# Kernel optimization log

Measured on AMD Instinct MI355X. Metric: run time of the kernel, lower is better.

Reference implementation:

```python
import jax, jax.numpy as jnp
import numpy as np

IN_DIM = 256
QK_DIM = IN_DIM // 8  # 32
NCLS = 19
B, H, W = 2, 64, 64


def conv3x3(x, w, b):
    # x: [B,C,H,W], w: [O,I,3,3] -> SAME padding, stride 1 (= pad=1 in torch)
    y = jax.lax.conv_general_dilated(x, w, (1, 1), 'SAME',
                                     dimension_numbers=('NCHW', 'OIHW', 'NCHW'))
    return y + b[None, :, None, None]


def setup_inputs() -> dict:
    key = jax.random.key(0)
    ks = jax.random.split(key, 20)
    s = 0.05
    inp = {
        'x': jax.random.normal(ks[0], (B, IN_DIM, H, W), jnp.float32),
        'modal_mask': jax.random.uniform(ks[1], (B, NCLS, H, W), jnp.float32),
        'amodal_mask': jax.random.uniform(ks[2], (B, NCLS, H, W), jnp.float32),
        'w_mp': jax.random.normal(ks[3], (NCLS, IN_DIM, 3, 3), jnp.float32) * s,
        'b_mp': jnp.zeros((NCLS,), jnp.float32),
        'w_ap': jax.random.normal(ks[4], (NCLS, IN_DIM, 3, 3), jnp.float32) * s,
        'b_ap': jnp.zeros((NCLS,), jnp.float32),
        'w_q': jax.random.normal(ks[5], (QK_DIM, IN_DIM + NCLS, 3, 3), jnp.float32) * s,
        'b_q': jnp.zeros((QK_DIM,), jnp.float32),
        'w_k': jax.random.normal(ks[6], (QK_DIM, IN_DIM + NCLS, 3, 3), jnp.float32) * s,
        'b_k': jnp.zeros((QK_DIM,), jnp.float32),
        'w_v': jax.random.normal(ks[7], (IN_DIM, IN_DIM, 3, 3), jnp.float32) * s,
        'b_v': jnp.zeros((IN_DIM,), jnp.float32),
        'w_comp': jax.random.normal(ks[8], (IN_DIM, IN_DIM + 2 * NCLS, 3, 3), jnp.float32) * s,
        'b_comp': jnp.zeros((IN_DIM,), jnp.float32),
        'w_out': jax.random.normal(ks[9], (IN_DIM, 3 * IN_DIM, 3, 3), jnp.float32) * s,
        'b_out': jnp.zeros((IN_DIM,), jnp.float32),
        # SELayer(in_dim, reduction=8): Linear(c, c//8, bias=False), Linear(c//8, c, bias=False)
        'w_se1': jax.random.normal(ks[10], (IN_DIM // 8, IN_DIM), jnp.float32) * s,
        'w_se2': jax.random.normal(ks[11], (IN_DIM, IN_DIM // 8), jnp.float32) * s,
    }
    return inp


def reference(x, modal_mask, amodal_mask, w_mp, b_mp, w_ap, b_ap, w_q, b_q,
              w_k, b_k, w_v, b_v, w_comp, b_comp, w_out, b_out, w_se1, w_se2):
    b, c, h, w = x.shape
    n = h * w
    # masks already at (h, w): nearest interpolate is identity
    modal_x = conv3x3(x, w_mp, b_mp) * modal_mask
    amodal_x = conv3x3(x, w_ap, b_ap) * amodal_mask
    inp = jnp.concatenate([x, modal_x, amodal_x], axis=1)
    out = conv3x3(inp, w_comp, b_comp)
    # SE layer
    y = out.mean(axis=(2, 3))                                # [b, c]
    y = jax.nn.sigmoid(jax.nn.relu(y @ w_se1.T) @ w_se2.T)   # [b, c]
    out_a = out * y[:, :, None, None]
    # dual-softmax spatial attention
    q = conv3x3(jnp.concatenate([x, modal_mask], axis=1), w_q, b_q).reshape(b, QK_DIM, n)
    k = conv3x3(jnp.concatenate([x, amodal_mask], axis=1), w_k, b_k).reshape(b, QK_DIM, n)
    v = conv3x3(x, w_v, b_v).reshape(b, c, n)
    energy = jnp.einsum('bdn,bdm->bnm', q, k)                # [b, n, n]
    attn = jax.nn.softmax(energy, axis=-1)                   # softmax over keys
    attn_t = jax.nn.softmax(energy, axis=1)                  # softmax over queries (of E^T rows)
    # out_b = bmm(v, attn^T); out_c = bmm(v, softmax(E^T,-1)^T)
    out_b = jnp.einsum('bcn,bmn->bcm', v, attn).reshape(b, c, h, w)
    out_c = jnp.einsum('bcn,bnm->bcm', v, attn_t).reshape(b, c, h, w)
    out = jnp.concatenate([out_a, out_b, out_c], axis=1)
    return conv3x3(out, w_out, b_out)
```

## Files before the change

kernel.cpp:

```cpp
#include <hip/hip_runtime.h>
#include <math.h>

#define HW 4096
#define IMG 64
#define PIX66 (66 * 66)

typedef short short8 __attribute__((ext_vector_type(8)));
typedef float f32x4 __attribute__((ext_vector_type(4)));

__device__ __forceinline__ unsigned short f2bf(float f) {
    unsigned int u = __float_as_uint(f);
    u += 0x7fff + ((u >> 16) & 1);
    return (unsigned short)(u >> 16);
}
__device__ __forceinline__ float bf2f(unsigned short h) {
    return __uint_as_float(((unsigned int)h) << 16);
}
__device__ __forceinline__ unsigned int pkbf(float a, float b) {
    unsigned int ua = __float_as_uint(a) + 0x8000u;
    unsigned int ub = __float_as_uint(b) + 0x8000u;
    return __builtin_amdgcn_perm(ub, ua, 0x07060302u);
}

__device__ __forceinline__ void gll16(const unsigned short* g, unsigned short* l) {
    __builtin_amdgcn_global_load_lds(
        (const __attribute__((address_space(1))) unsigned int*)(g),
        (__attribute__((address_space(3))) unsigned int*)(l), 16, 0, 0);
}

__device__ __forceinline__ int pxor(int pix) { return (pix ^ (pix >> 2)) & 3; }
__device__ __forceinline__ int p32o(int pix, int c) {
    return pix * 32 + ((((c >> 3) ^ pxor(pix)) & 3) << 3) + (c & 7);
}

struct WtJob {
    const float* w;
    unsigned short* dh;
    unsigned short* dl;
    int OC, OCpad, C0, K0pad, C1, Ktot;
};

__global__ __launch_bounds__(256) void k_wt_all(WtJob J0, WtJob J1, WtJob J2,
                                                WtJob J3, WtJob J4, WtJob J5,
                                                WtJob J6) {
    WtJob J;
    switch (blockIdx.y) {
        case 0: J = J0; break;
        case 1: J = J1; break;
        case 2: J = J2; break;
        case 3: J = J3; break;
        case 4: J = J4; break;
        case 5: J = J5; break;
        default: J = J6; break;
    }
    int idx = blockIdx.x * 256 + threadIdx.x;
    int KS = J.Ktot >> 5;
    int n = 9 * KS * J.OCpad * 32;
    if (idx >= n) return;
    int kk = idx & 31;
    int rest = idx >> 5;
    int oc = rest % J.OCpad;
    rest /= J.OCpad;
    int kg = rest % KS;
    int tap = rest / KS;
    int k = kg * 32 + kk;
    float v = 0.f;
    if (oc < J.OC) {
        int ic = -1;
        if (k < J.C0) ic = k;
        else if (k >= J.K0pad && (k - J.K0pad) < J.C1) ic = J.C0 + (k - J.K0pad);
        if (ic >= 0) v = J.w[((size_t)oc * (J.C0 + J.C1) + ic) * 9 + tap];
    }
    unsigned short hi = f2bf(v);
    J.dh[idx] = hi;
    if (J.dl) J.dl[idx] = f2bf(v - bf2f(hi));
}

__global__ __launch_bounds__(256) void k_build_x(const float* __restrict__ x,
                                                 unsigned short* __restrict__ xh,
                                                 unsigned short* __restrict__ xl,
                                                 unsigned short* __restrict__ ipad) {
    int b = blockIdx.z, c0 = blockIdx.y * 64, p0 = blockIdx.x * 64;
    __shared__ float s[64][65];
    int t = threadIdx.x;
    for (int i = t; i < 4096; i += 256) {
        int c = i >> 6, p = i & 63;
        s[p][c] = x[((size_t)b * 256 + c0 + c) * HW + p0 + p];
    }
    __syncthreads();
    for (int i = t; i < 4096; i += 256) {
        int c = i & 63, p = i >> 6;
        float f = s[p][c];
        unsigned short hi = f2bf(f);
        unsigned short lo = f2bf(f - bf2f(hi));
        int pp = p0 + p;
        int y = pp >> 6, xx = pp & 63;
        int pix = (y + 1) * 66 + xx + 1;
        int C = c0 + c;
        size_t ix = (size_t)(b * 8 + (C >> 5)) * (PIX66 * 32) + p32o(pix, C & 31);
        xh[ix] = hi;
        xl[ix] = lo;
        ipad[(size_t)(b * 10 + (C >> 5)) * (PIX66 * 32) + p32o(pix, C & 31)] = hi;
    }
}

__global__ __launch_bounds__(256) void k_build_mask2(
    const float* __restrict__ m0, const float* __restrict__ m1,
    unsigned short* __restrict__ d0h, unsigned short* __restrict__ d0l,
    unsigned short* __restrict__ d1h, unsigned short* __restrict__ d1l) {
    const float* m = blockIdx.y ? m1 : m0;
    unsigned short* dh = blockIdx.y ? d1h : d0h;
    unsigned short* dl = blockIdx.y ? d1l : d0l;
    int idx = blockIdx.x * 256 + threadIdx.x;
    int c = idx & 31;
    int p = (idx >> 5) & 4095;
    int b = idx >> 17;
    float f = (c < 19) ? m[((size_t)b * 19 + c) * HW + p] : 0.f;
    unsigned short hi = f2bf(f);
    int y = p >> 6, xx = p & 63;
    int pix = (y + 1) * 66 + xx + 1;
    dh[(size_t)b * (PIX66 * 32) + p32o(pix, c)] = hi;
    dl[(size_t)b * (PIX66 * 32) + p32o(pix, c)] = f2bf(f - bf2f(hi));
}

struct DJob {
    const unsigned short* s1h;
    const unsigned short* s1l;
    const unsigned short* wth;
    const unsigned short* wtl;
    const float* bias;
    unsigned short* d1;
    unsigned short* d2;
    const float* mask;
    int chBase;
    int mode;
    int split;
    int KS1;
};

__global__ __launch_bounds__(128, 2) void conv_direct_all(
    const unsigned short* __restrict__ s0h, const unsigned short* __restrict__ s0l,
    DJob j0, DJob j1, DJob j2, DJob j3) {
    DJob J;
    switch (blockIdx.y) {
        case 0: J = j0; break;
        case 1: J = j1; break;
        case 2: J = j2; break;
        default: J = j3; break;
    }
    const int KS0 = 8;
    int KS = KS0 + J.KS1;
    int ST = 9 * KS;
    int b = blockIdx.z;
    int t = threadIdx.x, w = t >> 6, l = t & 63, quad = l >> 4, ln = l & 15;
    int pBase = blockIdx.x * 64 + w * 32;

    int padpix[2];
#pragma unroll
    for (int tn = 0; tn < 2; ++tn) {
        int p = pBase + tn * 16 + ln;
        padpix[tn] = ((p >> 6) + 1) * 66 + (p & 63) + 1;
    }
    size_t aoff[2];
#pragma unroll
    for (int tm = 0; tm < 2; ++tm) aoff[tm] = (size_t)(tm * 16 + ln) * 32 + quad * 8;

    const unsigned short* S0H = s0h + (size_t)b * KS0 * PIX66 * 32;
    const unsigned short* S0L = s0l + (size_t)b * KS0 * PIX66 * 32;
    const unsigned short* S1H = J.KS1 ? J.s1h + (size_t)b * PIX66 * 32
                                      : (const unsigned short*)0;
    const unsigned short* S1L = J.KS1 ? J.s1l + (size_t)b * PIX66 * 32
                                      : (const unsigned short*)0;

    f32x4 acc[2][2];
#pragma unroll
    for (int i = 0; i < 2; ++i)
#pragma unroll
        for (int j = 0; j < 2; ++j) acc[i][j] = (f32x4){0.f, 0.f, 0.f, 0.f};

    int tap = 0, kg = 0;
    auto adv = [&]() { if (++kg == KS) { kg = 0; ++tap; } };
    auto loadStep = [&](int ltap, int lkg, short8* bh, short8* bl, short8* ah,
                        short8* al) {
        int d3 = ltap / 3;
        int dpix = (d3 - 1) * 66 + (ltap - d3 * 3 - 1);
        const unsigned short* SpH;
        const unsigned short* SpL;
        long plane;
        if (lkg < KS0) {
            SpH = S0H; SpL = S0L; plane = (long)lkg * PIX66 * 32;
        } else {
            SpH = S1H; SpL = S1L; plane = 0;
        }
#pragma unroll
        for (int tn = 0; tn < 2; ++tn) {
            int pix2 = padpix[tn] + dpix;
            long off = plane + (long)pix2 * 32 + (((quad ^ pxor(pix2)) & 3) << 3);
            bh[tn] = *(const short8*)(SpH + off);
            if (J.split) bl[tn] = *(const short8*)(SpL + off);
        }
        const unsigned short* WTh = J.wth + (size_t)(ltap * KS + lkg) * 32 * 32;
        ah[0] = *(const short8*)(WTh + aoff[0]);
        ah[1] = *(const short8*)(WTh + aoff[1]);
        if (J.split) {
            const unsigned short* WTl = J.wtl + (size_t)(ltap * KS + lkg) * 32 * 32;
            al[0] = *(const short8*)(WTl + aoff[0]);
            al[1] = *(const short8*)(WTl + aoff[1]);
        }
    };

    short8 BH[2][2], AH[2][2], BL[2][2], AL[2][2];
#pragma unroll
    for (int u = 0; u < 2; ++u) { loadStep(tap, kg, BH[u], BL[u], AH[u], AL[u]); adv(); }

    for (int s = 0; s < ST; s += 2) {
#pragma unroll
        for (int u = 0; u < 2; ++u) {
            if (s + u < ST) {
#pragma unroll
                for (int tm = 0; tm < 2; ++tm)
#pragma unroll
                    for (int tn = 0; tn < 2; ++tn) {
                        acc[tm][tn] = __builtin_amdgcn_mfma_f32_16x16x32_bf16(
                            AH[u][tm], BH[u][tn], acc[tm][tn], 0, 0, 0);
                        if (J.split) {
                            acc[tm][tn] = __builtin_amdgcn_mfma_f32_16x16x32_bf16(
                                AL[u][tm], BH[u][tn], acc[tm][tn], 0, 0, 0);
                            acc[tm][tn] = __builtin_amdgcn_mfma_f32_16x16x32_bf16(
                                AH[u][tm], BL[u][tn], acc[tm][tn], 0, 0, 0);
                        }
                    }
                if (s + u + 2 < ST) { loadStep(tap, kg, BH[u], BL[u], AH[u], AL[u]); adv(); }
            }
        }
    }

#pragma unroll
    for (int tm = 0; tm < 2; ++tm) {
#pragma unroll
        for (int r = 0; r < 4; ++r) {
            int oc = tm * 16 + quad * 4 + r;
#pragma unroll
            for (int tn = 0; tn < 2; ++tn) {
                int p = pBase + tn * 16 + ln;
                if (J.mode == 1) {
                    if (oc < 19) {
                        float v = (acc[tm][tn][r] + J.bias[oc]) *
                                  J.mask[((size_t)b * 19 + oc) * HW + p];
                        int ch = J.chBase + oc;
                        J.d1[(size_t)(b * 10 + (ch >> 5)) * (PIX66 * 32) +
                             p32o(padpix[tn], ch & 31)] = f2bf(v);
                    }
                } else {
                    float v = acc[tm][tn][r] + J.bias[oc];
                    unsigned short hi = f2bf(v);
                    J.d1[((size_t)b * HW + p) * 32 + oc] = hi;
                    J.d2[((size_t)b * HW + p) * 32 + oc] = f2bf(v - bf2f(hi));
                }
            }
        }
    }
}

struct LJob {
    const unsigned short* src;
    const unsigned short* wt;
    float* dstf;
    int KS;
    int nseg;
    int doSum;
};

__global__ __launch_bounds__(128, 3) void conv_lds(LJob j0, LJob j1, int ocgPerJob,
                                                   float* __restrict__ ybuf) {
    int jy = blockIdx.y;
    LJob J = (jy >= ocgPerJob) ? j1 : j0;
    int ocBase = ((jy >= ocgPerJob) ? jy - ocgPerJob : jy) * 64;
    int z = blockIdx.z;
    int b = z & 1, seg = z >> 1;
    int kgPer = J.KS / J.nseg;
    int kgBeg = seg * kgPer, kgEnd = kgBeg + kgPer;
    int ry = blockIdx.x * 2;
    int t = threadIdx.x, w = t >> 6, l = t & 63, quad = l >> 4, ln = l & 15;

    __shared__ unsigned short sB[2][264 * 32];

    const unsigned short* S = J.src + (size_t)b * J.KS * PIX66 * 32;
    const size_t bStageBase = (size_t)(ry * 66) * 32;

    f32x4 acc[4][4];
#pragma unroll
    for (int i = 0; i < 4; ++i)
#pragma unroll
        for (int j = 0; j < 4; ++j) acc[i][j] = (f32x4){0.f, 0.f, 0.f, 0.f};

    {
        const unsigned short* gB = S + (size_t)kgBeg * PIX66 * 32 + bStageBase;
        for (int i = t; i < 1056; i += 128) gll16(gB + (size_t)i * 8, sB[0] + (size_t)i * 8);
    }

    for (int kg = kgBeg; kg < kgEnd; ++kg) {
        int cur = (kg - kgBeg) & 1;
        __syncthreads();
        if (kg + 1 < kgEnd) {
            const unsigned short* gB = S + (size_t)(kg + 1) * PIX66 * 32 + bStageBase;
            for (int i = t; i < 1056; i += 128)
                gll16(gB + (size_t)i * 8, sB[cur ^ 1] + (size_t)i * 8);
        }
        const unsigned short* sBc = sB[cur];
#pragma unroll
        for (int tap = 0; tap < 9; ++tap) {
            const unsigned short* gA =
                J.wt + ((size_t)(tap * J.KS + kg) * 256 + ocBase) * 32;
            int dy = tap / 3 - 1, dx = tap % 3 - 1;
            int lpBase = (1 + w + dy) * 66 + 1 + dx;
            short8 bf[4], af[4];
#pragma unroll
            for (int tn = 0; tn < 4; ++tn) {
                int lp = lpBase + tn * 16 + ln;
                int P = ry * 66 + lp;
                bf[tn] = *(const short8*)(sBc + (size_t)lp * 32 +
                                          (((quad ^ pxor(P)) & 3) << 3));
            }
#pragma unroll
            for (int tm = 0; tm < 4; ++tm)
                af[tm] = *(const short8*)(gA + (size_t)(tm * 16 + ln) * 32 + quad * 8);
#pragma unroll
            for (int tm = 0; tm < 4; ++tm)
#pragma unroll
                for (int tn = 0; tn < 4; ++tn)
                    acc[tm][tn] = __builtin_amdgcn_mfma_f32_16x16x32_bf16(
                        af[tm], bf[tn], acc[tm][tn], 0, 0, 0);
        }
    }

    int prow = ry + w;
#pragma unroll
    for (int tm = 0; tm < 4; ++tm) {
#pragma unroll
        for (int r = 0; r < 4; ++r) {
            int oc = ocBase + tm * 16 + quad * 4 + r;
            float msum = 0.f;
#pragma unroll
            for (int tn = 0; tn < 4; ++tn) {
                int px = tn * 16 + ln;
                J.dstf[((size_t)z * 256 + oc) * HW + prow * 64 + px] = acc[tm][tn][r];
                msum += acc[tm][tn][r];
            }
            if (J.doSum) {
#pragma unroll
                for (int off = 8; off; off >>= 1) msum += __shfl_down(msum, off, 16);
                if (ln == 0) atomicAdd(&ybuf[b * 256 + oc], msum);
            }
        }
    }
}

__global__ __launch_bounds__(256) void vt_combine(const float* __restrict__ part,
                                                  const float* __restrict__ bias,
                                                  unsigned short* __restrict__ vt) {
    int idx = blockIdx.x * 256 + threadIdx.x;
    int p = idx & 4095;
    int oc = (idx >> 12) & 255;
    int b = idx >> 20;
    float v = part[((size_t)b * 256 + oc) * HW + p] +
              part[((size_t)(2 + b) * 256 + oc) * HW + p] + bias[oc];
    int prow = p >> 6, px = p & 63;
    int jc = ((px >> 3) ^ (oc & 7)) & 7;
    vt[(((size_t)b * 64 + prow) * 256 + oc) * 64 + jc * 8 + (px & 7)] = f2bf(v);
}

__global__ __launch_bounds__(256) void comp_combine(const float* __restrict__ part,
                                                    const float* __restrict__ bias,
                                                    const float* __restrict__ sc,
                                                    unsigned short* __restrict__ catN) {
    int idx = blockIdx.x * 256 + threadIdx.x;
    int p = idx & 4095;
    int oc = (idx >> 12) & 255;
    int b = idx >> 20;
    float v = (part[((size_t)b * 256 + oc) * HW + p] +
               part[((size_t)(2 + b) * 256 + oc) * HW + p] + bias[oc]) *
              sc[b * 256 + oc];
    int prow = p >> 6, px = p & 63;
    int pix = (prow + 1) * 66 + px + 1;
    catN[(size_t)(b * 24 + (oc >> 5)) * (PIX66 * 32) + p32o(pix, oc & 31)] = f2bf(v);
}

__global__ __launch_bounds__(256) void out_combine(const float* __restrict__ part,
                                                   const float* __restrict__ bias,
                                                   float* __restrict__ outp) {
    int idx = blockIdx.x * 256 + threadIdx.x;
    int p = idx & 4095;
    int oc = (idx >> 12) & 255;
    int b = idx >> 20;
    float v = part[((size_t)(0 + b) * 256 + oc) * HW + p] +
              part[((size_t)(2 + b) * 256 + oc) * HW + p] +
              part[((size_t)(4 + b) * 256 + oc) * HW + p] +
              part[((size_t)(6 + b) * 256 + oc) * HW + p] + bias[oc];
    outp[((size_t)b * 256 + oc) * HW + p] = v;
}

__global__ __launch_bounds__(512, 4) void flash_attn(
    const unsigned short* __restrict__ qt_h, const unsigned short* __restrict__ qt_l,
    const unsigned short* __restrict__ kt_h, const unsigned short* __restrict__ kt_l,
    const unsigned short* __restrict__ vt,
    float* __restrict__ pO, float* __restrict__ pm, float* __restrict__ pl) {
    int seg = blockIdx.y >> 1, mode = blockIdx.y & 1, b = blockIdx.z;
    size_t qkoff = (size_t)b * HW * 32;
    const unsigned short* Qh = (mode ? kt_h : qt_h) + qkoff;
    const unsigned short* Ql = (mode ? kt_l : qt_l) + qkoff;
    const unsigned short* Kh = (mode ? qt_h : kt_h) + qkoff;
    const unsigned short* Kl = (mode ? qt_l : kt_l) + qkoff;
    const unsigned short* Vt = vt + (size_t)b * 64 * 256 * 64;

    int t = threadIdx.x, w = t >> 6, l = t & 63, quad = l >> 4, ln = l & 15;
    int pg = w & 1, ch = w >> 1;
    int p0 = blockIdx.x * 64, pw = pg * 32;
    int cb = ch * 64;
    bool soft = (ch == (pg ? 3 : 0));

    __shared__ unsigned short sV[256 * 64];
    __shared__ unsigned short sP[64 * 68];
    __shared__ float sAl[64];

    short8 qbh[2], qbl[2];
    if (soft) {
#pragma unroll
        for (int pn = 0; pn < 2; ++pn) {
            size_t off = (size_t)(p0 + pw + pn * 16 + ln) * 32 + quad * 8;
            qbh[pn] = *(const short8*)(Qh + off);
            qbl[pn] = *(const short8*)(Ql + off);
        }
    }

    float m_run[2] = {-3.0e38f, -3.0e38f};
    float l_run[2] = {0.f, 0.f};
    f32x4 accO[4][2];
#pragma unroll
    for (int cs = 0; cs < 4; ++cs)
#pragma unroll
        for (int pn = 0; pn < 2; ++pn) accO[cs][pn] = (f32x4){0.f, 0.f, 0.f, 0.f};

    int jbBeg = seg * (HW / 2);
    for (int jb = jbBeg; jb < jbBeg + HW / 2; jb += 64) {
        __syncthreads();
        {
            const unsigned short* gV = Vt + (size_t)(jb >> 6) * (256 * 64);
#pragma unroll
            for (int i = 0; i < 4; ++i)
                gll16(gV + (size_t)(t + 512 * i) * 8, sV + (size_t)(t + 512 * i) * 8);
        }
        if (soft) {
            f32x4 sacc[2][4];
#pragma unroll
            for (int pn = 0; pn < 2; ++pn)
#pragma unroll
                for (int jj = 0; jj < 4; ++jj) sacc[pn][jj] = (f32x4){0.f, 0.f, 0.f, 0.f};
#pragma unroll
            for (int jj = 0; jj < 4; ++jj) {
                size_t off = (size_t)(jb + 16 * jj + ln) * 32 + quad * 8;
                short8 kh = *(const short8*)(Kh + off);
                short8 kr = *(const short8*)(Kl + off);
#pragma unroll
                for (int pn = 0; pn < 2; ++pn) {
                    sacc[pn][jj] = __builtin_amdgcn_mfma_f32_16x16x32_bf16(
                        kh, qbh[pn], sacc[pn][jj], 0, 0, 0);
                    sacc[pn][jj] = __builtin_amdgcn_mfma_f32_16x16x32_bf16(
                        kh, qbl[pn], sacc[pn][jj], 0, 0, 0);
                    sacc[pn][jj] = __builtin_amdgcn_mfma_f32_16x16x32_bf16(
                        kr, qbh[pn], sacc[pn][jj], 0, 0, 0);
                }
            }
#pragma unroll
            for (int pn = 0; pn < 2; ++pn) {
                float tmx = -3.0e38f;
#pragma unroll
                for (int jj = 0; jj < 4; ++jj)
#pragma unroll
                    for (int r = 0; r < 4; ++r) tmx = fmaxf(tmx, sacc[pn][jj][r]);
                tmx = fmaxf(tmx, __shfl_xor(tmx, 16));
                tmx = fmaxf(tmx, __shfl_xor(tmx, 32));
                float mnew = fmaxf(m_run[pn], tmx);
                float alpha = __expf(m_run[pn] - mnew);
                m_run[pn] = mnew;
                float psum = 0.f;
#pragma unroll
                for (int jj = 0; jj < 4; ++jj) {
                    float e0 = __expf(sacc[pn][jj][0] - mnew);
                    float e1 = __expf(sacc[pn][jj][1] - mnew);
                    float e2 = __expf(sacc[pn][jj][2] - mnew);
                    float e3 = __expf(sacc[pn][jj][3] - mnew);
                    psum += (e0 + e1) + (e2 + e3);
                    uint2 pk;
                    pk.x = pkbf(e0, e1);
                    pk.y = pkbf(e2, e3);
                    *(uint2*)(sP + (size_t)(pw + pn * 16 + ln) * 68 + jj * 16 +
                              quad * 4) = pk;
                }
                psum += __shfl_xor(psum, 16);
                psum += __shfl_xor(psum, 32);
                l_run[pn] = l_run[pn] * alpha + psum;
                if (quad == 0) sAl[pw + pn * 16 + ln] = alpha;
            }
        }
        __syncthreads();
        float al0 = sAl[pw + ln];
        float al1 = sAl[pw + 16 + ln];
#pragma unroll
        for (int cs = 0; cs < 4; ++cs) { accO[cs][0] *= al0; accO[cs][1] *= al1; }
#pragma unroll
        for (int j2 = 0; j2 < 2; ++j2) {
            short8 pb0 = *(const short8*)(sP + (size_t)(pw + ln) * 68 + j2 * 32 +
                                          quad * 8);
            short8 pb1 = *(const short8*)(sP + (size_t)(pw + 16 + ln) * 68 + j2 * 32 +
                                          quad * 8);
#pragma unroll
            for (int cs = 0; cs < 4; ++cs) {
                int c = cb + cs * 16 + ln;
                short8 va = *(const short8*)(
                    sV + (size_t)c * 64 + ((((j2 * 4 + quad) ^ (c & 7)) & 7) << 3));
                accO[cs][0] = __builtin_amdgcn_mfma_f32_16x16x32_bf16(
                    va, pb0, accO[cs][0], 0, 0, 0);
                accO[cs][1] = __builtin_amdgcn_mfma_f32_16x16x32_bf16(
                    va, pb1, accO[cs][1], 0, 0, 0);
            }
        }
    }

    int idx4 = (seg * 2 + mode) * 2 + b;
#pragma unroll
    for (int pn = 0; pn < 2; ++pn) {
        int p = p0 + pw + pn * 16 + ln;
        if (soft && quad == 0) {
            pm[(size_t)idx4 * HW + p] = m_run[pn];
            pl[(size_t)idx4 * HW + p] = l_run[pn];
        }
#pragma unroll
        for (int cs = 0; cs < 4; ++cs)
#pragma unroll
            for (int r = 0; r < 4; ++r) {
                int c = cb + cs * 16 + quad * 4 + r;
                pO[((size_t)idx4 * 256 + c) * HW + p] = accO[cs][pn][r];
            }
    }
}

__global__ __launch_bounds__(256) void attn_combine(const float* __restrict__ pO,
                                                    const float* __restrict__ pm,
                                                    const float* __restrict__ pl,
                                                    unsigned short* __restrict__ catN) {
    int b = blockIdx.z, mode = blockIdx.y;
    int t = threadIdx.x;
    int p = blockIdx.x * 64 + (t & 63);
    int c0 = (t >> 6) * 64;
    int i0 = mode * 2 + b;
    int i1 = 4 + mode * 2 + b;
    float m0 = pm[(size_t)i0 * HW + p], m1 = pm[(size_t)i1 * HW + p];
    float l0 = pl[(size_t)i0 * HW + p], l1 = pl[(size_t)i1 * HW + p];
    float M = fmaxf(m0, m1);
    float e0 = __expf(m0 - M), e1 = __expf(m1 - M);
    float inv = 1.f / (l0 * e0 + l1 * e1);
    e0 *= inv;
    e1 *= inv;
    int y = p >> 6, x = p & 63;
    int pix = (y + 1) * 66 + x + 1;
    for (int c = c0; c < c0 + 64; ++c) {
        float v = pO[((size_t)i0 * 256 + c) * HW + p] * e0 +
                  pO[((size_t)i1 * 256 + c) * HW + p] * e1;
        int cf = 256 + mode * 256 + c;
        catN[(size_t)(b * 24 + (cf >> 5)) * (PIX66 * 32) + p32o(pix, cf & 31)] = f2bf(v);
    }
}

__global__ __launch_bounds__(256) void se_mlp_kernel(const float* __restrict__ y,
                                                     const float* __restrict__ bcomp,
                                                     const float* __restrict__ w1,
                                                     const float* __restrict__ w2,
                                                     float* __restrict__ sc) {
    int b = blockIdx.x, t = threadIdx.x;
    __shared__ float sy[256], sh[32];
    sy[t] = y[b * 256 + t] * (1.f / 4096.f) + bcomp[t];
    __syncthreads();
    if (t < 32) {
        float s = 0.f;
        for (int c = 0; c < 256; ++c) s = fmaf(w1[t * 256 + c], sy[c], s);
        sh[t] = fmaxf(s, 0.f);
    }
    __syncthreads();
    float s = 0.f;
#pragma unroll
    for (int h = 0; h < 32; ++h) s = fmaf(w2[t * 32 + h], sh[h], s);
    sc[b * 256 + t] = 1.f / (1.f + __expf(-s));
}

extern "C" void kernel_launch(void* const* d_in, const int* in_sizes, int n_in,
                              void* d_out, int out_size, void* d_ws, size_t ws_size,
                              hipStream_t stream) {
    const float* x      = (const float*)d_in[0];
    const float* mmask  = (const float*)d_in[1];
    const float* amask  = (const float*)d_in[2];
    const float* w_mp   = (const float*)d_in[3];
    const float* b_mp   = (const float*)d_in[4];
    const float* w_ap   = (const float*)d_in[5];
    const float* b_ap   = (const float*)d_in[6];
    const float* w_q    = (const float*)d_in[7];
    const float* b_q    = (const float*)d_in[8];
    const float* w_k    = (const float*)d_in[9];
    const float* b_k    = (const float*)d_in[10];
    const float* w_v    = (const float*)d_in[11];
    const float* b_v    = (const float*)d_in[12];
    const float* w_comp = (const float*)d_in[13];
    const float* b_comp = (const float*)d_in[14];
    const float* w_out  = (const float*)d_in[15];
    const float* b_out  = (const float*)d_in[16];
    const float* w_se1  = (const float*)d_in[17];
    const float* w_se2  = (const float*)d_in[18];

    unsigned short* us = (unsigned short*)d_ws;
    size_t o = 0;
    unsigned short* xpad_hi = us + o; o += (size_t)2 * 8 * PIX66 * 32;
    unsigned short* xpad_lo = us + o; o += (size_t)2 * 8 * PIX66 * 32;
    unsigned short* mq_hi   = us + o; o += (size_t)2 * PIX66 * 32;
    unsigned short* mq_lo   = us + o; o += (size_t)2 * PIX66 * 32;
    unsigned short* ma_hi   = us + o; o += (size_t)2 * PIX66 * 32;
    unsigned short* ma_lo   = us + o; o += (size_t)2 * PIX66 * 32;
    unsigned short* ipad    = us + o; o += (size_t)2 * 10 * PIX66 * 32;
    unsigned short* catN    = us + o; o += (size_t)2 * 24 * PIX66 * 32;
    size_t zeroBytes = o * sizeof(unsigned short);
    unsigned short* wt_mp = us + o; o += (size_t)9 * 8 * 32 * 32;
    unsigned short* wt_ap = us + o; o += (size_t)9 * 8 * 32 * 32;
    unsigned short* wt_qh = us + o; o += (size_t)9 * 9 * 32 * 32;
    unsigned short* wt_ql = us + o; o += (size_t)9 * 9 * 32 * 32;
    unsigned short* wt_kh = us + o; o += (size_t)9 * 9 * 32 * 32;
    unsigned short* wt_kl = us + o; o += (size_t)9 * 9 * 32 * 32;
    unsigned short* wt_v  = us + o; o += (size_t)9 * 8 * 256 * 32;
    unsigned short* wt_cp = us + o; o += (size_t)9 * 10 * 256 * 32;
    unsigned short* wt_ot = us + o; o += (size_t)9 * 24 * 256 * 32;
    unsigned short* qt_h  = us + o; o += (size_t)2 * HW * 32;
    unsigned short* qt_l  = us + o; o += (size_t)2 * HW * 32;
    unsigned short* kt_h  = us + o; o += (size_t)2 * HW * 32;
    unsigned short* kt_l  = us + o; o += (size_t)2 * HW * 32;
    unsigned short* vt    = us + o; o += (size_t)2 * 64 * 256 * 64;
    float* fp = (float*)(us + o);
    size_t fo = 0;
    float* pAtt = fp + fo; fo += (size_t)8 * 256 * HW;
    float* pmb  = fp + fo; fo += (size_t)8 * HW;
    float* plb  = fp + fo; fo += (size_t)8 * HW;
    float* pOut = fp + fo; fo += (size_t)8 * 256 * HW;
    float* pV   = fp + fo; fo += (size_t)4 * 256 * HW;
    float* pC   = fp + fo; fo += (size_t)4 * 256 * HW;
    float* ybuf = fp + fo; fo += 512;
    float* sbuf = fp + fo; fo += 512;
    size_t need = o * sizeof(unsigned short) + fo * sizeof(float);
    if (ws_size < need) return;

    float* outp = (float*)d_out;

    hipMemsetAsync(us, 0, zeroBytes, stream);
    hipMemsetAsync(ybuf, 0, 512 * sizeof(float), stream);

    WtJob W0{w_mp,   wt_mp, (unsigned short*)0, 19, 32, 256, 256, 0, 256};
    WtJob W1{w_ap,   wt_ap, (unsigned short*)0, 19, 32, 256, 256, 0, 256};
    WtJob W2{w_q,    wt_qh, wt_ql,             32, 32, 256, 256, 19, 288};
    WtJob W3{w_k,    wt_kh, wt_kl,             32, 32, 256, 256, 19, 288};
    WtJob W4{w_v,    wt_v,  (unsigned short*)0, 256, 256, 256, 256, 0, 256};
    WtJob W5{w_comp, wt_cp, (unsigned short*)0, 256, 256, 294, 320, 0, 320};
    WtJob W6{w_out,  wt_ot, (unsigned short*)0, 256, 256, 768, 768, 0, 768};
    k_wt_all<<<dim3((9 * 24 * 256 * 32 + 255) / 256, 7), 256, 0, stream>>>(
        W0, W1, W2, W3, W4, W5, W6);

    k_build_x<<<dim3(64, 4, 2), 256, 0, stream>>>(x, xpad_hi, xpad_lo, ipad);
    k_build_mask2<<<dim3(1024, 2), 256, 0, stream>>>(mmask, amask, mq_hi, mq_lo,
                                                     ma_hi, ma_lo);

    const unsigned short* NUS = (const unsigned short*)0;
    unsigned short* NUSo = (unsigned short*)0;
    float* NF = (float*)0;

    DJob dm{NUS, NUS, wt_mp, NUS, b_mp, ipad, NUSo, mmask, 256, 1, 0, 0};
    DJob da{NUS, NUS, wt_ap, NUS, b_ap, ipad, NUSo, amask, 275, 1, 0, 0};
    DJob dq{mq_hi, mq_lo, wt_qh, wt_ql, b_q, qt_h, qt_l, NF, 0, 2, 1, 1};
    DJob dk{ma_hi, ma_lo, wt_kh, wt_kl, b_k, kt_h, kt_l, NF, 0, 2, 1, 1};
    conv_direct_all<<<dim3(64, 4, 2), 128, 0, stream>>>(xpad_hi, xpad_lo, dm, da, dq, dk);

    LJob lv{xpad_hi, wt_v, pV, 8, 2, 0};
    LJob lc{ipad, wt_cp, pC, 10, 2, 1};
    conv_lds<<<dim3(32, 8, 4), 128, 0, stream>>>(lv, lc, 4, ybuf);

    se_mlp_kernel<<<2, 256, 0, stream>>>(ybuf, b_comp, w_se1, w_se2, sbuf);
    vt_combine<<<8192, 256, 0, stream>>>(pV, b_v, vt);
    comp_combine<<<8192, 256, 0, stream>>>(pC, b_comp, sbuf, catN);

    flash_attn<<<dim3(64, 4, 2), 512, 0, stream>>>(qt_h, qt_l, kt_h, kt_l, vt,
                                                   pAtt, pmb, plb);
    attn_combine<<<dim3(64, 2, 2), 256, 0, stream>>>(pAtt, pmb, plb, catN);

    LJob lo{catN, wt_ot, pOut, 24, 4, 0};
    conv_lds<<<dim3(32, 4, 8), 128, 0, stream>>>(lo, lo, 4, NF);
    out_combine<<<8192, 256, 0, stream>>>(pOut, b_out, outp);
}
```

Measured before the change: 424.2 us.

## Pipeline flash attention with dedicated softmax warps and double-buffered P

The flash attention kernel now uses the two softmax warps purely as producers. They compute QK scores and probabilities for the next key tile into a double-buffered sP/sAl while the other six warps run the PV MFMAs on the current tile, with the 256 channels split 96/80/80 across them. This is meant to overlap the exp/softmax work with the PV matmul instead of serialising them, at the cost of more accumulator registers (6 tiles) and an extra barrier per iteration. Separately, the V and comp combine kernels are merged into one launch to save a kernel launch and share index math.

After: 444.3 us. 1.05x slower.

```diff
diff --git a/kernel.cpp b/kernel.cpp
--- a/kernel.cpp
+++ b/kernel.cpp
@@ -356,34 +356,25 @@
     }
 }
 
-__global__ __launch_bounds__(256) void vt_combine(const float* __restrict__ part,
-                                                  const float* __restrict__ bias,
-                                                  unsigned short* __restrict__ vt) {
+__global__ __launch_bounds__(256) void vc_combine(
+    const float* __restrict__ pV, const float* __restrict__ bv,
+    unsigned short* __restrict__ vt,
+    const float* __restrict__ pC, const float* __restrict__ bc,
+    const float* __restrict__ sc, unsigned short* __restrict__ catN) {
     int idx = blockIdx.x * 256 + threadIdx.x;
     int p = idx & 4095;
     int oc = (idx >> 12) & 255;
     int b = idx >> 20;
-    float v = part[((size_t)b * 256 + oc) * HW + p] +
-              part[((size_t)(2 + b) * 256 + oc) * HW + p] + bias[oc];
     int prow = p >> 6, px = p & 63;
+    float v = pV[((size_t)b * 256 + oc) * HW + p] +
+              pV[((size_t)(2 + b) * 256 + oc) * HW + p] + bv[oc];
     int jc = ((px >> 3) ^ (oc & 7)) & 7;
     vt[(((size_t)b * 64 + prow) * 256 + oc) * 64 + jc * 8 + (px & 7)] = f2bf(v);
-}
-
-__global__ __launch_bounds__(256) void comp_combine(const float* __restrict__ part,
-                                                    const float* __restrict__ bias,
-                                                    const float* __restrict__ sc,
-                                                    unsigned short* __restrict__ catN) {
-    int idx = blockIdx.x * 256 + threadIdx.x;
-    int p = idx & 4095;
-    int oc = (idx >> 12) & 255;
-    int b = idx >> 20;
-    float v = (part[((size_t)b * 256 + oc) * HW + p] +
-               part[((size_t)(2 + b) * 256 + oc) * HW + p] + bias[oc]) *
+    float c = (pC[((size_t)b * 256 + oc) * HW + p] +
+               pC[((size_t)(2 + b) * 256 + oc) * HW + p] + bc[oc]) *
               sc[b * 256 + oc];
-    int prow = p >> 6, px = p & 63;
     int pix = (prow + 1) * 66 + px + 1;
-    catN[(size_t)(b * 24 + (oc >> 5)) * (PIX66 * 32) + p32o(pix, oc & 31)] = f2bf(v);
+    catN[(size_t)(b * 24 + (oc >> 5)) * (PIX66 * 32) + p32o(pix, oc & 31)] = f2bf(c);
 }
 
 __global__ __launch_bounds__(256) void out_combine(const float* __restrict__ part,
@@ -416,12 +407,14 @@
     int t = threadIdx.x, w = t >> 6, l = t & 63, quad = l >> 4, ln = l & 15;
     int pg = w & 1, ch = w >> 1;
     int p0 = blockIdx.x * 64, pw = pg * 32;
-    int cb = ch * 64;
     bool soft = (ch == (pg ? 3 : 0));
+    int s = pg ? ch : (ch - 1);
+    int ncs = (s == 0) ? 6 : 5;
+    int cb = (s == 0) ? 0 : (96 + (s - 1) * 80);
 
     __shared__ unsigned short sV[256 * 64];
-    __shared__ unsigned short sP[64 * 68];
-    __shared__ float sAl[64];
+    __shared__ unsigned short sP[2][64 * 68];
+    __shared__ float sAl[2][64];
 
     short8 qbh[2], qbl[2];
     if (soft) {
@@ -435,113 +428,136 @@
 
     float m_run[2] = {-3.0e38f, -3.0e38f};
     float l_run[2] = {0.f, 0.f};
-    f32x4 accO[4][2];
-#pragma unroll
-    for (int cs = 0; cs < 4; ++cs)
-#pragma unroll
-        for (int pn = 0; pn < 2; ++pn) accO[cs][pn] = (f32x4){0.f, 0.f, 0.f, 0.f};
+    f32x4 accO[6][2];
+#pragma unroll
+    for (int cs = 0; cs < 6; ++cs) {
+        accO[cs][0] = (f32x4){0.f, 0.f, 0.f, 0.f};
+        accO[cs][1] = (f32x4){0.f, 0.f, 0.f, 0.f};
+    }
 
     int jbBeg = seg * (HW / 2);
-    for (int jb = jbBeg; jb < jbBeg + HW / 2; jb += 64) {
+    const int NT = (HW / 2) / 64;
+
+    auto qkstep = [&](int it2) {
+        int jb = jbBeg + it2 * 64;
+        int nb = it2 & 1;
+        f32x4 sacc[2][4];
+#pragma unroll
+        for (int pn = 0; pn < 2; ++pn)
+#pragma unroll
+            for (int jj = 0; jj < 4; ++jj) sacc[pn][jj] = (f32x4){0.f, 0.f, 0.f, 0.f};
+#pragma unroll
+        for (int jj = 0; jj < 4; ++jj) {
+            size_t off = (size_t)(jb + 16 * jj + ln) * 32 + quad * 8;
+            short8 kh = *(const short8*)(Kh + off);
+            short8 kr = *(const short8*)(Kl + off);
+#pragma unroll
+            for (int pn = 0; pn < 2; ++pn) {
+                sacc[pn][jj] = __builtin_amdgcn_mfma_f32_16x16x32_bf16(
+                    kh, qbh[pn], sacc[pn][jj], 0, 0, 0);
+                sacc[pn][jj] = __builtin_amdgcn_mfma_f32_16x16x32_bf16(
+                    kh, qbl[pn], sacc[pn][jj], 0, 0, 0);
+                sacc[pn][jj] = __builtin_amdgcn_mfma_f32_16x16x32_bf16(
+                    kr, qbh[pn], sacc[pn][jj], 0, 0, 0);
+            }
+        }
+#pragma unroll
+        for (int pn = 0; pn < 2; ++pn) {
+            float tmx = -3.0e38f;
+#pragma unroll
+            for (int jj = 0; jj < 4; ++jj)
+#pragma unroll
+                for (int r = 0; r < 4; ++r) tmx = fmaxf(tmx, sacc[pn][jj][r]);
+            tmx = fmaxf(tmx, __shfl_xor(tmx, 16));
+            tmx = fmaxf(tmx, __shfl_xor(tmx, 32));
+            float mnew = fmaxf(m_run[pn], tmx);
+            float alpha = __expf(m_run[pn] - mnew);
+            m_run[pn] = mnew;
+            float psum = 0.f;
+#pragma unroll
+            for (int jj = 0; jj < 4; ++jj) {
+                float e0 = __expf(sacc[pn][jj][0] - mnew);
+                float e1 = __expf(sacc[pn][jj][1] - mnew);
+                float e2 = __expf(sacc[pn][jj][2] - mnew);
+                float e3 = __expf(sacc[pn][jj][3] - mnew);
+                psum += (e0 + e1) + (e2 + e3);
+                uint2 pk;
+                pk.x = pkbf(e0, e1);
+                pk.y = pkbf(e2, e3);
+                *(uint2*)(sP[nb] + (size_t)(pw + pn * 16 + ln) * 68 + jj * 16 +
+                          quad * 4) = pk;
+            }
+            psum += __shfl_xor(psum, 16);
+            psum += __shfl_xor(psum, 32);
+            l_run[pn] = l_run[pn] * alpha + psum;
+            if (quad == 0) sAl[nb][pw + pn * 16 + ln] = alpha;
+        }
+    };
+
+    if (soft) qkstep(0);
+
+    for (int it = 0; it < NT; ++it) {
+        int cur = it & 1;
         __syncthreads();
         {
-            const unsigned short* gV = Vt + (size_t)(jb >> 6) * (256 * 64);
+            const unsigned short* gV = Vt + (size_t)((jbBeg >> 6) + it) * (256 * 64);
 #pragma unroll
             for (int i = 0; i < 4; ++i)
                 gll16(gV + (size_t)(t + 512 * i) * 8, sV + (size_t)(t + 512 * i) * 8);
         }
+        __syncthreads();
         if (soft) {
-            f32x4 sacc[2][4];
-#pragma unroll
-            for (int pn = 0; pn < 2; ++pn)
-#pragma unroll
-                for (int jj = 0; jj < 4; ++jj) sacc[pn][jj] = (f32x4){0.f, 0.f, 0.f, 0.f};
-#pragma unroll
-            for (int jj = 0; jj < 4; ++jj) {
-                size_t off = (size_t)(jb + 16 * jj + ln) * 32 + quad * 8;
-                short8 kh = *(const short8*)(Kh + off);
-                short8 kr = *(const short8*)(Kl + off);
-#pragma unroll
-                for (int pn = 0; pn < 2; ++pn) {
-                    sacc[pn][jj] = __builtin_amdgcn_mfma_f32_16x16x32_bf16(
-                        kh, qbh[pn], sacc[pn][jj], 0, 0, 0);
-                    sacc[pn][jj] = __builtin_amdgcn_mfma_f32_16x16x32_bf16(
-                        kh, qbl[pn], sacc[pn][jj], 0, 0, 0);
-                    sacc[pn][jj] = __builtin_amdgcn_mfma_f32_16x16x32_bf16(
-                        kr, qbh[pn], sacc[pn][jj], 0, 0, 0);
-                }
-            }
+            if (it + 1 < NT) qkstep(it + 1);
+        } else {
+            float a0 = sAl[cur][pw + ln], a1 = sAl[cur][pw + 16 + ln];
+#pragma unroll
+            for (int cs = 0; cs < 6; ++cs)
+                if (cs < ncs) { accO[cs][0] *= a0; accO[cs][1] *= a1; }
+#pragma unroll
+            for (int j2 = 0; j2 < 2; ++j2) {
+                short8 pb0 = *(const short8*)(sP[cur] + (size_t)(pw + ln) * 68 +
+                                              j2 * 32 + quad * 8);
+                short8 pb1 = *(const short8*)(sP[cur] + (size_t)(pw + 16 + ln) * 68 +
+                                              j2 * 32 + quad * 8);
+#pragma unroll
+                for (int cs = 0; cs < 6; ++cs)
+                    if (cs < ncs) {
+                        int c = cb + cs * 16 + ln;
+                        short8 va = *(const short8*)(
+                            sV + (size_t)c * 64 +
+                            ((((j2 * 4 + quad) ^ (c & 7)) & 7) << 3));
+                        accO[cs][0] = __builtin_amdgcn_mfma_f32_16x16x32_bf16(
+                            va, pb0, accO[cs][0], 0, 0, 0);
+                        accO[cs][1] = __builtin_amdgcn_mfma_f32_16x16x32_bf16(
+                            va, pb1, accO[cs][1], 0, 0, 0);
+                    }
+            }
+        }
+    }
+
+    int idx4 = (seg * 2 + mode) * 2 + b;
+    if (soft) {
+        if (quad == 0) {
 #pragma unroll
             for (int pn = 0; pn < 2; ++pn) {
-                float tmx = -3.0e38f;
-#pragma unroll
-                for (int jj = 0; jj < 4; ++jj)
-#pragma unroll
-                    for (int r = 0; r < 4; ++r) tmx = fmaxf(tmx, sacc[pn][jj][r]);
-                tmx = fmaxf(tmx, __shfl_xor(tmx, 16));
-                tmx = fmaxf(tmx, __shfl_xor(tmx, 32));
-                float mnew = fmaxf(m_run[pn], tmx);
-                float alpha = __expf(m_run[pn] - mnew);
-                m_run[pn] = mnew;
-                float psum = 0.f;
-#pragma unroll
-                for (int jj = 0; jj < 4; ++jj) {
-                    float e0 = __expf(sacc[pn][jj][0] - mnew);
-                    float e1 = __expf(sacc[pn][jj][1] - mnew);
-                    float e2 = __expf(sacc[pn][jj][2] - mnew);
-                    float e3 = __expf(sacc[pn][jj][3] - mnew);
-                    psum += (e0 + e1) + (e2 + e3);
-                    uint2 pk;
-                    pk.x = pkbf(e0, e1);
-                    pk.y = pkbf(e2, e3);
-                    *(uint2*)(sP + (size_t)(pw + pn * 16 + ln) * 68 + jj * 16 +
-                              quad * 4) = pk;
-                }
-                psum += __shfl_xor(psum, 16);
-                psum += __shfl_xor(psum, 32);
-                l_run[pn] = l_run[pn] * alpha + psum;
-                if (quad == 0) sAl[pw + pn * 16 + ln] = alpha;
-            }
-        }
-        __syncthreads();
-        float al0 = sAl[pw + ln];
-        float al1 = sAl[pw + 16 + ln];
-#pragma unroll
-        for (int cs = 0; cs < 4; ++cs) { accO[cs][0] *= al0; accO[cs][1] *= al1; }
-#pragma unroll
-        for (int j2 = 0; j2 < 2; ++j2) {
-            short8 pb0 = *(const short8*)(sP + (size_t)(pw + ln) * 68 + j2 * 32 +
-                                          quad * 8);
-            short8 pb1 = *(const short8*)(sP + (size_t)(pw + 16 + ln) * 68 + j2 * 32 +
-                                          quad * 8);
-#pragma unroll
-            for (int cs = 0; cs < 4; ++cs) {
-                int c = cb + cs * 16 + ln;
-                short8 va = *(const short8*)(
-                    sV + (size_t)c * 64 + ((((j2 * 4 + quad) ^ (c & 7)) & 7) << 3));
-                accO[cs][0] = __builtin_amdgcn_mfma_f32_16x16x32_bf16(
-                    va, pb0, accO[cs][0], 0, 0, 0);
-                accO[cs][1] = __builtin_amdgcn_mfma_f32_16x16x32_bf16(
-                    va, pb1, accO[cs][1], 0, 0, 0);
-            }
-        }
-    }
-
-    int idx4 = (seg * 2 + mode) * 2 + b;
-#pragma unroll
-    for (int pn = 0; pn < 2; ++pn) {
-        int p = p0 + pw + pn * 16 + ln;
-        if (soft && quad == 0) {
-            pm[(size_t)idx4 * HW + p] = m_run[pn];
-            pl[(size_t)idx4 * HW + p] = l_run[pn];
-        }
-#pragma unroll
-        for (int cs = 0; cs < 4; ++cs)
-#pragma unroll
-            for (int r = 0; r < 4; ++r) {
-                int c = cb + cs * 16 + quad * 4 + r;
-                pO[((size_t)idx4 * 256 + c) * HW + p] = accO[cs][pn][r];
-            }
+                int p = p0 + pw + pn * 16 + ln;
+                pm[(size_t)idx4 * HW + p] = m_run[pn];
+                pl[(size_t)idx4 * HW + p] = l_run[pn];
+            }
+        }
+    } else {
+#pragma unroll
+        for (int pn = 0; pn < 2; ++pn) {
+            int p = p0 + pw + pn * 16 + ln;
+#pragma unroll
+            for (int cs = 0; cs < 6; ++cs)
+                if (cs < ncs)
+#pragma unroll
+                    for (int r = 0; r < 4; ++r) {
+                        int c = cb + cs * 16 + quad * 4 + r;
+                        pO[((size_t)idx4 * 256 + c) * HW + p] = accO[cs][pn][r];
+                    }
+        }
     }
 }
 
@@ -688,8 +704,7 @@
     conv_lds<<<dim3(32, 8, 4), 128, 0, stream>>>(lv, lc, 4, ybuf);
 
     se_mlp_kernel<<<2, 256, 0, stream>>>(ybuf, b_comp, w_se1, w_se2, sbuf);
-    vt_combine<<<8192, 256, 0, stream>>>(pV, b_v, vt);
-    comp_combine<<<8192, 256, 0, stream>>>(pC, b_comp, sbuf, catN);
+    vc_combine<<<8192, 256, 0, stream>>>(pV, b_v, vt, pC, b_comp, sbuf, catN);
 
     flash_attn<<<dim3(64, 4, 2), 512, 0, stream>>>(qt_h, qt_l, kt_h, kt_l, vt,
                                                    pAtt, pmb, plb);
```

## Split flash attention channels across blocks with dedicated softmax waves; fuse combines

Applied to the files above, without the earlier changes.

Flash attention now splits the 256 V channels into two halves across separate blocks. Each block runs 6 waves: per pixel group, one wave does only the QK/softmax and two waves do only the PV MMAs. This doubles the grid and halves V shared memory, so more blocks fit per CU, at the cost of computing the softmax twice. The V and comp combine kernels are also merged into one launch.

New measurement: 614.4 us. +44.8%, slower.

```diff
diff --git a/kernel.cpp b/kernel.cpp
--- a/kernel.cpp
+++ b/kernel.cpp
@@ -356,34 +356,25 @@
     }
 }
 
-__global__ __launch_bounds__(256) void vt_combine(const float* __restrict__ part,
-                                                  const float* __restrict__ bias,
-                                                  unsigned short* __restrict__ vt) {
+__global__ __launch_bounds__(256) void vc_combine(
+    const float* __restrict__ pV, const float* __restrict__ bv,
+    unsigned short* __restrict__ vt,
+    const float* __restrict__ pC, const float* __restrict__ bc,
+    const float* __restrict__ sc, unsigned short* __restrict__ catN) {
     int idx = blockIdx.x * 256 + threadIdx.x;
     int p = idx & 4095;
     int oc = (idx >> 12) & 255;
     int b = idx >> 20;
-    float v = part[((size_t)b * 256 + oc) * HW + p] +
-              part[((size_t)(2 + b) * 256 + oc) * HW + p] + bias[oc];
     int prow = p >> 6, px = p & 63;
+    float v = pV[((size_t)b * 256 + oc) * HW + p] +
+              pV[((size_t)(2 + b) * 256 + oc) * HW + p] + bv[oc];
     int jc = ((px >> 3) ^ (oc & 7)) & 7;
     vt[(((size_t)b * 64 + prow) * 256 + oc) * 64 + jc * 8 + (px & 7)] = f2bf(v);
-}
-
-__global__ __launch_bounds__(256) void comp_combine(const float* __restrict__ part,
-                                                    const float* __restrict__ bias,
-                                                    const float* __restrict__ sc,
-                                                    unsigned short* __restrict__ catN) {
-    int idx = blockIdx.x * 256 + threadIdx.x;
-    int p = idx & 4095;
-    int oc = (idx >> 12) & 255;
-    int b = idx >> 20;
-    float v = (part[((size_t)b * 256 + oc) * HW + p] +
-               part[((size_t)(2 + b) * 256 + oc) * HW + p] + bias[oc]) *
+    float c = (pC[((size_t)b * 256 + oc) * HW + p] +
+               pC[((size_t)(2 + b) * 256 + oc) * HW + p] + bc[oc]) *
               sc[b * 256 + oc];
-    int prow = p >> 6, px = p & 63;
     int pix = (prow + 1) * 66 + px + 1;
-    catN[(size_t)(b * 24 + (oc >> 5)) * (PIX66 * 32) + p32o(pix, oc & 31)] = f2bf(v);
+    catN[(size_t)(b * 24 + (oc >> 5)) * (PIX66 * 32) + p32o(pix, oc & 31)] = f2bf(c);
 }
 
 __global__ __launch_bounds__(256) void out_combine(const float* __restrict__ part,
@@ -400,26 +391,30 @@
     outp[((size_t)b * 256 + oc) * HW + p] = v;
 }
 
-__global__ __launch_bounds__(512, 4) void flash_attn(
+__global__ __launch_bounds__(384, 6) void flash_attn(
     const unsigned short* __restrict__ qt_h, const unsigned short* __restrict__ qt_l,
     const unsigned short* __restrict__ kt_h, const unsigned short* __restrict__ kt_l,
     const unsigned short* __restrict__ vt,
     float* __restrict__ pO, float* __restrict__ pm, float* __restrict__ pl) {
-    int seg = blockIdx.y >> 1, mode = blockIdx.y & 1, b = blockIdx.z;
+    int yy = blockIdx.y;
+    int chh = yy & 1, mode = (yy >> 1) & 1, seg = yy >> 2;
+    int b = blockIdx.z;
     size_t qkoff = (size_t)b * HW * 32;
     const unsigned short* Qh = (mode ? kt_h : qt_h) + qkoff;
     const unsigned short* Ql = (mode ? kt_l : qt_l) + qkoff;
     const unsigned short* Kh = (mode ? qt_h : kt_h) + qkoff;
     const unsigned short* Kl = (mode ? qt_l : kt_l) + qkoff;
-    const unsigned short* Vt = vt + (size_t)b * 64 * 256 * 64;
-
-    int t = threadIdx.x, w = t >> 6, l = t & 63, quad = l >> 4, ln = l & 15;
-    int pg = w & 1, ch = w >> 1;
+    const unsigned short* Vt =
+        vt + (size_t)b * 64 * 256 * 64 + (size_t)chh * 128 * 64;
+
+    int t = threadIdx.x, w = t / 64, l = t & 63, quad = l >> 4, ln = l & 15;
+    int pg = (w >= 3) ? 1 : 0;
+    int wi = w - pg * 3;
+    bool soft = (wi == 0);
     int p0 = blockIdx.x * 64, pw = pg * 32;
-    int cb = ch * 64;
-    bool soft = (ch == (pg ? 3 : 0));
-
-    __shared__ unsigned short sV[256 * 64];
+    int cbl = (wi - 1) * 64;
+
+    __shared__ unsigned short sV[128 * 64];
     __shared__ unsigned short sP[64 * 68];
     __shared__ float sAl[64];
 
@@ -437,18 +432,18 @@
     float l_run[2] = {0.f, 0.f};
     f32x4 accO[4][2];
 #pragma unroll
-    for (int cs = 0; cs < 4; ++cs)
-#pragma unroll
-        for (int pn = 0; pn < 2; ++pn) accO[cs][pn] = (f32x4){0.f, 0.f, 0.f, 0.f};
+    for (int cs = 0; cs < 4; ++cs) {
+        accO[cs][0] = (f32x4){0.f, 0.f, 0.f, 0.f};
+        accO[cs][1] = (f32x4){0.f, 0.f, 0.f, 0.f};
+    }
 
     int jbBeg = seg * (HW / 2);
     for (int jb = jbBeg; jb < jbBeg + HW / 2; jb += 64) {
         __syncthreads();
         {
             const unsigned short* gV = Vt + (size_t)(jb >> 6) * (256 * 64);
-#pragma unroll
-            for (int i = 0; i < 4; ++i)
-                gll16(gV + (size_t)(t + 512 * i) * 8, sV + (size_t)(t + 512 * i) * 8);
+            for (int i = t; i < 1024; i += 384)
+                gll16(gV + (size_t)i * 8, sV + (size_t)i * 8);
         }
         if (soft) {
             f32x4 sacc[2][4];
@@ -504,44 +499,53 @@
             }
         }
         __syncthreads();
-        float al0 = sAl[pw + ln];
-        float al1 = sAl[pw + 16 + ln];
-#pragma unroll
-        for (int cs = 0; cs < 4; ++cs) { accO[cs][0] *= al0; accO[cs][1] *= al1; }
-#pragma unroll
-        for (int j2 = 0; j2 < 2; ++j2) {
-            short8 pb0 = *(const short8*)(sP + (size_t)(pw + ln) * 68 + j2 * 32 +
-                                          quad * 8);
-            short8 pb1 = *(const short8*)(sP + (size_t)(pw + 16 + ln) * 68 + j2 * 32 +
-                                          quad * 8);
-#pragma unroll
-            for (int cs = 0; cs < 4; ++cs) {
-                int c = cb + cs * 16 + ln;
-                short8 va = *(const short8*)(
-                    sV + (size_t)c * 64 + ((((j2 * 4 + quad) ^ (c & 7)) & 7) << 3));
-                accO[cs][0] = __builtin_amdgcn_mfma_f32_16x16x32_bf16(
-                    va, pb0, accO[cs][0], 0, 0, 0);
-                accO[cs][1] = __builtin_amdgcn_mfma_f32_16x16x32_bf16(
-                    va, pb1, accO[cs][1], 0, 0, 0);
+        if (!soft) {
+            float al0 = sAl[pw + ln];
+            float al1 = sAl[pw + 16 + ln];
+#pragma unroll
+            for (int cs = 0; cs < 4; ++cs) { accO[cs][0] *= al0; accO[cs][1] *= al1; }
+#pragma unroll
+            for (int j2 = 0; j2 < 2; ++j2) {
+                short8 pb0 = *(const short8*)(sP + (size_t)(pw + ln) * 68 + j2 * 32 +
+                                              quad * 8);
+                short8 pb1 = *(const short8*)(sP + (size_t)(pw + 16 + ln) * 68 +
+                                              j2 * 32 + quad * 8);
+#pragma unroll
+                for (int cs = 0; cs < 4; ++cs) {
+                    int c = cbl + cs * 16 + ln;
+                    short8 va = *(const short8*)(
+                        sV + (size_t)c * 64 + ((((j2 * 4 + quad) ^ (c & 7)) & 7) << 3));
+                    accO[cs][0] = __builtin_amdgcn_mfma_f32_16x16x32_bf16(
+                        va, pb0, accO[cs][0], 0, 0, 0);
+                    accO[cs][1] = __builtin_amdgcn_mfma_f32_16x16x32_bf16(
+                        va, pb1, accO[cs][1], 0, 0, 0);
+                }
             }
         }
     }
 
     int idx4 = (seg * 2 + mode) * 2 + b;
-#pragma unroll
-    for (int pn = 0; pn < 2; ++pn) {
-        int p = p0 + pw + pn * 16 + ln;
-        if (soft && quad == 0) {
-            pm[(size_t)idx4 * HW + p] = m_run[pn];
-            pl[(size_t)idx4 * HW + p] = l_run[pn];
-        }
-#pragma unroll
-        for (int cs = 0; cs < 4; ++cs)
-#pragma unroll
-            for (int r = 0; r < 4; ++r) {
-                int c = cb + cs * 16 + quad * 4 + r;
-                pO[((size_t)idx4 * 256 + c) * HW + p] = accO[cs][pn][r];
-            }
+    if (soft) {
+        if (chh == 0 && quad == 0) {
+#pragma unroll
+            for (int pn = 0; pn < 2; ++pn) {
+                int p = p0 + pw + pn * 16 + ln;
+                pm[(size_t)idx4 * HW + p] = m_run[pn];
+                pl[(size_t)idx4 * HW + p] = l_run[pn];
+            }
+        }
+    } else {
+#pragma unroll
+        for (int pn = 0; pn < 2; ++pn) {
+            int p = p0 + pw + pn * 16 + ln;
+#pragma unroll
+            for (int cs = 0; cs < 4; ++cs)
+#pragma unroll
+                for (int r = 0; r < 4; ++r) {
+                    int c = chh * 128 + cbl + cs * 16 + quad * 4 + r;
+                    pO[((size_t)idx4 * 256 + c) * HW + p] = accO[cs][pn][r];
+                }
+        }
     }
 }
 
@@ -688,10 +692,9 @@
     conv_lds<<<dim3(32, 8, 4), 128, 0, stream>>>(lv, lc, 4, ybuf);
 
     se_mlp_kernel<<<2, 256, 0, stream>>>(ybuf, b_comp, w_se1, w_se2, sbuf);
-    vt_combine<<<8192, 256, 0, stream>>>(pV, b_v, vt);
-    comp_combine<<<8192, 256, 0, stream>>>(pC, b_comp, sbuf, catN);
-
-    flash_attn<<<dim3(64, 4, 2), 512, 0, stream>>>(qt_h, qt_l, kt_h, kt_l, vt,
+    vc_combine<<<8192, 256, 0, stream>>>(pV, b_v, vt, pC, b_comp, sbuf, catN);
+
+    flash_attn<<<dim3(64, 8, 2), 384, 0, stream>>>(qt_h, qt_l, kt_h, kt_l, vt,
                                                    pAtt, pmb, plb);
     attn_combine<<<dim3(64, 2, 2), 256, 0, stream>>>(pAtt, pmb, plb, catN);
 
```

## Split flash attention keys into four segments and fuse V/comp combine kernels

Applied to the files above, without the earlier changes.

Flash attention now splits the key range into four segments instead of two, doubling the grid in y, and attn_combine merges four partial softmax states. The V and comp combine kernels are fused into one launch, and the attention and output partial buffers share one allocation. The aim is more parallelism in the attention stage and one fewer launch, at the cost of writing and reading twice as much partial output traffic.

After: 424.6 us. Within noise of the previous version (+0.1%).

```diff
diff --git a/kernel.cpp b/kernel.cpp
--- a/kernel.cpp
+++ b/kernel.cpp
@@ -356,34 +356,25 @@
     }
 }
 
-__global__ __launch_bounds__(256) void vt_combine(const float* __restrict__ part,
-                                                  const float* __restrict__ bias,
-                                                  unsigned short* __restrict__ vt) {
+__global__ __launch_bounds__(256) void vc_combine(
+    const float* __restrict__ pV, const float* __restrict__ bv,
+    unsigned short* __restrict__ vt,
+    const float* __restrict__ pC, const float* __restrict__ bc,
+    const float* __restrict__ sc, unsigned short* __restrict__ catN) {
     int idx = blockIdx.x * 256 + threadIdx.x;
     int p = idx & 4095;
     int oc = (idx >> 12) & 255;
     int b = idx >> 20;
-    float v = part[((size_t)b * 256 + oc) * HW + p] +
-              part[((size_t)(2 + b) * 256 + oc) * HW + p] + bias[oc];
     int prow = p >> 6, px = p & 63;
+    float v = pV[((size_t)b * 256 + oc) * HW + p] +
+              pV[((size_t)(2 + b) * 256 + oc) * HW + p] + bv[oc];
     int jc = ((px >> 3) ^ (oc & 7)) & 7;
     vt[(((size_t)b * 64 + prow) * 256 + oc) * 64 + jc * 8 + (px & 7)] = f2bf(v);
-}
-
-__global__ __launch_bounds__(256) void comp_combine(const float* __restrict__ part,
-                                                    const float* __restrict__ bias,
-                                                    const float* __restrict__ sc,
-                                                    unsigned short* __restrict__ catN) {
-    int idx = blockIdx.x * 256 + threadIdx.x;
-    int p = idx & 4095;
-    int oc = (idx >> 12) & 255;
-    int b = idx >> 20;
-    float v = (part[((size_t)b * 256 + oc) * HW + p] +
-               part[((size_t)(2 + b) * 256 + oc) * HW + p] + bias[oc]) *
+    float c = (pC[((size_t)b * 256 + oc) * HW + p] +
+               pC[((size_t)(2 + b) * 256 + oc) * HW + p] + bc[oc]) *
               sc[b * 256 + oc];
-    int prow = p >> 6, px = p & 63;
     int pix = (prow + 1) * 66 + px + 1;
-    catN[(size_t)(b * 24 + (oc >> 5)) * (PIX66 * 32) + p32o(pix, oc & 31)] = f2bf(v);
+    catN[(size_t)(b * 24 + (oc >> 5)) * (PIX66 * 32) + p32o(pix, oc & 31)] = f2bf(c);
 }
 
 __global__ __launch_bounds__(256) void out_combine(const float* __restrict__ part,
@@ -441,8 +432,8 @@
 #pragma unroll
         for (int pn = 0; pn < 2; ++pn) accO[cs][pn] = (f32x4){0.f, 0.f, 0.f, 0.f};
 
-    int jbBeg = seg * (HW / 2);
-    for (int jb = jbBeg; jb < jbBeg + HW / 2; jb += 64) {
+    int jbBeg = seg * (HW / 4);
+    for (int jb = jbBeg; jb < jbBeg + HW / 4; jb += 64) {
         __syncthreads();
         {
             const unsigned short* gV = Vt + (size_t)(jb >> 6) * (256 * 64);
@@ -553,20 +544,33 @@
     int t = threadIdx.x;
     int p = blockIdx.x * 64 + (t & 63);
     int c0 = (t >> 6) * 64;
-    int i0 = mode * 2 + b;
-    int i1 = 4 + mode * 2 + b;
-    float m0 = pm[(size_t)i0 * HW + p], m1 = pm[(size_t)i1 * HW + p];
-    float l0 = pl[(size_t)i0 * HW + p], l1 = pl[(size_t)i1 * HW + p];
-    float M = fmaxf(m0, m1);
-    float e0 = __expf(m0 - M), e1 = __expf(m1 - M);
-    float inv = 1.f / (l0 * e0 + l1 * e1);
-    e0 *= inv;
-    e1 *= inv;
+    int is[4];
+    float mm[4], ll[4];
+    float M = -3.0e38f;
+#pragma unroll
+    for (int s = 0; s < 4; ++s) {
+        is[s] = (s * 2 + mode) * 2 + b;
+        mm[s] = pm[(size_t)is[s] * HW + p];
+        ll[s] = pl[(size_t)is[s] * HW + p];
+        M = fmaxf(M, mm[s]);
+    }
+    float den = 0.f;
+    float e[4];
+#pragma unroll
+    for (int s = 0; s < 4; ++s) {
+        e[s] = __expf(mm[s] - M);
+        den += ll[s] * e[s];
+    }
+    float inv = 1.f / den;
+#pragma unroll
+    for (int s = 0; s < 4; ++s) e[s] *= inv;
     int y = p >> 6, x = p & 63;
     int pix = (y + 1) * 66 + x + 1;
     for (int c = c0; c < c0 + 64; ++c) {
-        float v = pO[((size_t)i0 * 256 + c) * HW + p] * e0 +
-                  pO[((size_t)i1 * 256 + c) * HW + p] * e1;
+        float v = 0.f;
+#pragma unroll
+        for (int s = 0; s < 4; ++s)
+            v += pO[((size_t)is[s] * 256 + c) * HW + p] * e[s];
         int cf = 256 + mode * 256 + c;
         catN[(size_t)(b * 24 + (cf >> 5)) * (PIX66 * 32) + p32o(pix, cf & 31)] = f2bf(v);
     }
@@ -643,16 +647,17 @@
     unsigned short* vt    = us + o; o += (size_t)2 * 64 * 256 * 64;
     float* fp = (float*)(us + o);
     size_t fo = 0;
-    float* pAtt = fp + fo; fo += (size_t)8 * 256 * HW;
-    float* pmb  = fp + fo; fo += (size_t)8 * HW;
-    float* plb  = fp + fo; fo += (size_t)8 * HW;
-    float* pOut = fp + fo; fo += (size_t)8 * 256 * HW;
+    float* pBig = fp + fo; fo += (size_t)16 * 256 * HW;
+    float* pmb  = fp + fo; fo += (size_t)16 * HW;
+    float* plb  = fp + fo; fo += (size_t)16 * HW;
     float* pV   = fp + fo; fo += (size_t)4 * 256 * HW;
     float* pC   = fp + fo; fo += (size_t)4 * 256 * HW;
     float* ybuf = fp + fo; fo += 512;
     float* sbuf = fp + fo; fo += 512;
     size_t need = o * sizeof(unsigned short) + fo * sizeof(float);
     if (ws_size < need) return;
+    float* pAtt = pBig;
+    float* pOut = pBig;
 
     float* outp = (float*)d_out;
 
@@ -688,10 +693,9 @@
     conv_lds<<<dim3(32, 8, 4), 128, 0, stream>>>(lv, lc, 4, ybuf);
 
     se_mlp_kernel<<<2, 256, 0, stream>>>(ybuf, b_comp, w_se1, w_se2, sbuf);
-    vt_combine<<<8192, 256, 0, stream>>>(pV, b_v, vt);
-    comp_combine<<<8192, 256, 0, stream>>>(pC, b_comp, sbuf, catN);
-
-    flash_attn<<<dim3(64, 4, 2), 512, 0, stream>>>(qt_h, qt_l, kt_h, kt_l, vt,
+    vc_combine<<<8192, 256, 0, stream>>>(pV, b_v, vt, pC, b_comp, sbuf, catN);
+
+    flash_attn<<<dim3(64, 8, 2), 512, 0, stream>>>(qt_h, qt_l, kt_h, kt_l, vt,
                                                    pAtt, pmb, plb);
     attn_combine<<<dim3(64, 2, 2), 256, 0, stream>>>(pAtt, pmb, plb, catN);
 
```
